# Optimization experiments

Measured on AMD Instinct MI355X. Metric: run time of the kernel, lower is better.

Reference implementation:

```python
import jax, jax.numpy as jnp
import numpy as np

B, C, H, W = 8, 128, 96, 96
E = 8           # num_experts
K = 3           # active_experts
HID = 4 * C     # hidden dim of each expert (hidden_ratio=4)


def _conv1x1(x, w, b):
    # x: [B,C,H,W], w: [O,C], b: [O] -> [B,O,H,W]
    return jnp.einsum('bchw,oc->bohw', x, w) + b[None, :, None, None]


def setup_inputs() -> dict:
    key = jax.random.key(0)
    ks = jax.random.split(key, 12)
    s = lambda k, shape, fan_in: jax.random.normal(k, shape, jnp.float32) * (1.0 / np.sqrt(fan_in))
    return {
        'x':   jax.random.normal(ks[0], (B, C, H, W), jnp.float32),
        # shared expert: Conv2d(C->HID,1x1), GELU, Conv2d(HID->C,1x1)
        'sw1': s(ks[1], (HID, C), C),   'sb1': jnp.zeros((HID,), jnp.float32),
        'sw2': s(ks[2], (C, HID), HID), 'sb2': jnp.zeros((C,), jnp.float32),
        # router gate: Conv2d(C->E,1x1)
        'gw':  s(ks[3], (E, C), C),     'gb':  jnp.zeros((E,), jnp.float32),
        # stacked routed experts
        'ew1': s(ks[4], (E, HID, C), C),   'eb1': jnp.zeros((E, HID), jnp.float32),
        'ew2': s(ks[5], (E, C, HID), HID), 'eb2': jnp.zeros((E, C), jnp.float32),
    }


def reference(x, sw1, sb1, sw2, sb2, gw, gb, ew1, eb1, ew2, eb2):
    # shared expert (exact GELU, matching torch nn.GELU default)
    h_s = jax.nn.gelu(_conv1x1(x, sw1, sb1), approximate=False)
    shared_out = _conv1x1(h_s, sw2, sb2)

    # router: softmax over expert dim, top-k, renormalize
    logits = _conv1x1(x, gw, gb)                      # [B,E,H,W]
    scores = jax.nn.softmax(logits, axis=1)           # [B,E,H,W]
    s_last = jnp.transpose(scores, (0, 2, 3, 1))      # [B,H,W,E]
    topk_probs, topk_idx = jax.lax.top_k(s_last, K)   # [B,H,W,K]
    topk_probs = topk_probs / jnp.sum(topk_probs, axis=-1, keepdims=True)

    # expert_mask[b,e,h,w]: routing weight for expert e at location (scatter-equivalent)
    onehot = jax.nn.one_hot(topk_idx, E, dtype=x.dtype)        # [B,H,W,K,E]
    mask = jnp.einsum('bhwke,bhwk->behw', onehot, topk_probs)  # [B,E,H,W]

    # dense compute of all experts (faithful to original), masked combine
    h = jax.nn.gelu(jnp.einsum('bchw,eoc->beohw', x, ew1)
                    + eb1[None, :, :, None, None], approximate=False)  # [B,E,HID,H,W]
    y = jnp.einsum('beohw,eco->bechw', h, ew2) + eb2[None, :, :, None, None]
    moe_out = jnp.einsum('bechw,behw->bchw', y, mask)

    # load-balancing aux loss
    mean_prob = jnp.mean(scores, axis=(0, 2, 3))               # [E]
    mean_load = jnp.mean(jnp.sum(onehot, axis=3), axis=(0, 1, 2))  # [E]
    aux_loss = E * jnp.sum(mean_prob * mean_load)

    return (x + shared_out + moe_out, aux_loss)
```

## Files before the change

### kernel.cpp

```cpp
#include <hip/hip_runtime.h>


typedef __bf16 bf16x8 __attribute__((ext_vector_type(8)));
typedef unsigned short u16x8 __attribute__((ext_vector_type(8)));
typedef float f32x4 __attribute__((ext_vector_type(4)));

#define HWP 9216
#define NPIX 73728
#define LDX 136
#define LDH 136
#define LXP 68
#define MAXSLOTS 77312
#define MAXTILES 1208
#define NSH 16

__device__ __forceinline__ unsigned short f2bf(float f) {
    unsigned u = __float_as_uint(f);
    u += 0x7fffu + ((u >> 16) & 1u);
    return (unsigned short)(u >> 16);
}

__device__ __forceinline__ unsigned pk_bf16(float a, float b) {
    return (unsigned)f2bf(a) | ((unsigned)f2bf(b) << 16);
}

__device__ __forceinline__ float bf2f(unsigned short h) {
    return __uint_as_float((unsigned)h << 16);
}

__device__ __forceinline__ float fast_gelu(float x) {
    float x2 = x * x;
    float u = x * fmaf(0.0356774081f, x2, 0.7978845608f);
    float e = __builtin_amdgcn_exp2f(u * 2.8853900818f);
    float r = __builtin_amdgcn_rcpf(e + 1.0f);
    float t = fmaf(-2.0f, r, 1.0f);
    float s = 0.5f * x;
    return fmaf(s, t, s);
}

__device__ __forceinline__ f32x4 mfma16(u16x8 a, u16x8 b, f32x4 c) {
    return __builtin_amdgcn_mfma_f32_16x16x32_bf16(
        __builtin_bit_cast(bf16x8, a), __builtin_bit_cast(bf16x8, b), c, 0, 0, 0);
}

__global__ __launch_bounds__(256) void router_fused(
    const float* __restrict__ x, const float* __restrict__ gw,
    const float* __restrict__ gb,
    const float* __restrict__ sw1, const float* __restrict__ sw2,
    const float* __restrict__ ew1, const float* __restrict__ ew2,
    unsigned short* __restrict__ wbf,
    unsigned short* __restrict__ xT,
    int* __restrict__ pixmask, float* __restrict__ pixw3,
    int* __restrict__ pixaux,
    int* __restrict__ bincount, float* __restrict__ accum)
{
    __shared__ float gws[1024];
    __shared__ float xls[128 * LXP];
    __shared__ float part[4 * 64 * 8];

    const int tid = threadIdx.x;
    const int blk = blockIdx.x;
    const int shadow = blk & (NSH - 1);

    {
        int i = blk * 256 + tid;
        #pragma unroll
        for (int j = 0; j < 4; ++j) {
            float v;
            if (i < 65536) v = sw1[i];
            else if (i < 131072) v = sw2[i - 65536];
            else if (i < 655360) v = ew1[i - 131072];
            else v = ew2[i - 655360];
            wbf[i] = f2bf(v);
            i += 1152 * 256;
        }
    }

    for (int i = tid; i < 1024; i += 256) gws[i] = gw[i];

    const int b = blk / 144;
    const int p0 = (blk - b * 144) * 64;
    const float* xb = x + (size_t)b * 128 * HWP + p0;

    #pragma unroll
    for (int j = 0; j < 8; ++j) {
        int id4 = j * 256 + tid;
        int c = id4 >> 4;
        int g = id4 & 15;
        f32x4 v = *(const f32x4*)(xb + (size_t)c * HWP + g * 4);
        *(f32x4*)&xls[c * LXP + g * 4] = v;
    }
    __syncthreads();

    const int p = tid & 63, q = tid >> 6;
    {
        float lg[8];
        #pragma unroll
        for (int e = 0; e < 8; ++e) lg[e] = 0.f;
        #pragma unroll
        for (int k = 0; k < 32; ++k) {
            int c = q * 32 + k;
            float xv = xls[c * LXP + p];
            #pragma unroll
            for (int e = 0; e < 8; ++e) lg[e] = fmaf(xv, gws[e * 128 + c], lg[e]);
        }
        #pragma unroll
        for (int e = 0; e < 8; ++e) part[(q * 64 + p) * 8 + e] = lg[e];
    }
    __syncthreads();

    if (tid < 64) {
        const int gp = b * HWP + p0 + tid;
        float l2[8];
        #pragma unroll
        for (int e = 0; e < 8; ++e)
            l2[e] = gb[e] + part[tid * 8 + e] + part[(64 + tid) * 8 + e]
                  + part[(128 + tid) * 8 + e] + part[(192 + tid) * 8 + e];
        float mx = l2[0];
        #pragma unroll
        for (int e = 1; e < 8; ++e) mx = fmaxf(mx, l2[e]);
        float pr[8]; float s = 0.f;
        #pragma unroll
        for (int e = 0; e < 8; ++e) { pr[e] = __expf(l2[e] - mx); s += pr[e]; }
        float sinv = __builtin_amdgcn_rcpf(s);
        #pragma unroll
        for (int e = 0; e < 8; ++e) pr[e] *= sinv;

        unsigned chosen = 0; float topsum = 0.f;
        for (int k = 0; k < 3; ++k) {
            int best = 0; float bv = -1.f;
            #pragma unroll
            for (int e = 0; e < 8; ++e) {
                bool ok = !((chosen >> e) & 1u) && pr[e] > bv;
                bv = ok ? pr[e] : bv;
                best = ok ? e : best;
            }
            chosen |= 1u << best;
            topsum += bv;
        }
        float tinv = __builtin_amdgcn_rcpf(topsum);

        pixmask[gp] = (int)chosen;
        {
            int j = 0;
            #pragma unroll
            for (int e = 0; e < 8; ++e)
                if ((chosen >> e) & 1u) { pixw3[gp * 3 + j] = pr[e] * tinv; ++j; }
        }

        unsigned long long eq = ~0ull;
        #pragma unroll
        for (int bit = 0; bit < 8; ++bit) {
            unsigned long long bb = __ballot((chosen >> bit) & 1u);
            eq &= ((chosen >> bit) & 1u) ? bb : ~bb;
        }
        const unsigned long long lowmask = (tid == 0) ? 0ull : (~0ull >> (64 - tid));
        int rank = __popcll(eq & lowmask);
        int cnt = __popcll(eq);
        int leader = __ffsll((unsigned long long)eq) - 1;
        int off_val = 0;
        if (rank == 0) off_val = atomicAdd(&bincount[shadow * 256 + (int)chosen], cnt);
        int binoff = __shfl(off_val, leader);
        pixaux[gp] = binoff + rank;

        #pragma unroll
        for (int e = 0; e < 8; ++e) {
            float v = pr[e];
            float c2 = ((chosen >> e) & 1u) ? 1.f : 0.f;
            #pragma unroll
            for (int off = 32; off > 0; off >>= 1) {
                v += __shfl_down(v, off);
                c2 += __shfl_down(c2, off);
            }
            if (tid == 0) {
                atomicAdd(&accum[shadow * 16 + e], v);
                atomicAdd(&accum[shadow * 16 + 8 + e], c2);
            }
        }
    }

    {
        const int pp = tid >> 2, qq = tid & 3;
        unsigned short* dst = xT + ((size_t)(blk * 64 + pp)) * 128 + qq * 32;
        #pragma unroll
        for (int j = 0; j < 4; ++j) {
            const int c0 = qq * 32 + j * 8;
            uint4 wv;
            wv.x = pk_bf16(xls[(c0 + 0) * LXP + pp], xls[(c0 + 1) * LXP + pp]);
            wv.y = pk_bf16(xls[(c0 + 2) * LXP + pp], xls[(c0 + 3) * LXP + pp]);
            wv.z = pk_bf16(xls[(c0 + 4) * LXP + pp], xls[(c0 + 5) * LXP + pp]);
            wv.w = pk_bf16(xls[(c0 + 6) * LXP + pp], xls[(c0 + 7) * LXP + pp]);
            *(uint4*)(dst + j * 8) = wv;
        }
    }
}

__global__ __launch_bounds__(256) void fill_bins(
    const int* __restrict__ bincount, const int* __restrict__ pixmask,
    int* __restrict__ idx, int* __restrict__ pixaux,
    int* __restrict__ tileMask, int* __restrict__ tileBase,
    int* __restrict__ ntiles)
{
    __shared__ int spc[256], snt[256], bb[256];
    __shared__ int sbase[NSH][256];
    const int tid = threadIdx.x;
    int c = 0;
    #pragma unroll
    for (int s = 0; s < NSH; ++s) {
        sbase[s][tid] = c;
        c += bincount[s * 256 + tid];
    }
    const int nt = (c + 63) >> 6;
    const int pc = nt << 6;
    spc[tid] = pc; snt[tid] = nt;
    __syncthreads();
    #pragma unroll
    for (int off = 1; off < 256; off <<= 1) {
        int a = (tid >= off) ? spc[tid - off] : 0;
        int d = (tid >= off) ? snt[tid - off] : 0;
        __syncthreads();
        spc[tid] += a; snt[tid] += d;
        __syncthreads();
    }
    const int base = spc[tid] - pc;
    bb[tid] = base;
    if (blockIdx.x == 0) {
        const int tstart = snt[tid] - nt;
        for (int j = 0; j < nt; ++j) {
            tileMask[tstart + j] = tid;
            tileBase[tstart + j] = base + (j << 6);
        }
        if (tid == 255) ntiles[0] = snt[255];
    }
    __syncthreads();

    const int gp = blockIdx.x * 256 + tid;
    int mask = pixmask[gp];
    int shadow = (gp >> 6) & (NSH - 1);
    int slot = bb[mask] + sbase[shadow][mask] + pixaux[gp];
    idx[slot] = gp;
    pixaux[gp] = slot;
}

__global__ __launch_bounds__(256, 3) void moe_sparse(
    const unsigned short* __restrict__ xT, const int* __restrict__ idx,
    const float* __restrict__ pixw3,
    const int* __restrict__ tileMask, const int* __restrict__ tileBase,
    const int* __restrict__ ntiles,
    const unsigned short* __restrict__ wbf,
    const float* __restrict__ sb1, const float* __restrict__ sb2,
    const float* __restrict__ eb1, const float* __restrict__ eb2,
    unsigned short* __restrict__ outT)
{
    __shared__ unsigned short xs[64 * LDX];
    __shared__ unsigned short hs[64 * LDH];
    __shared__ float wls[64 * 4];

    const int t = blockIdx.x;
    if (t >= ntiles[0]) return;
    const int mask = tileMask[t];
    const int base = tileBase[t];
    const int tid = threadIdx.x;

    {
        const int p = tid >> 2, q = tid & 3;
        const int gp = idx[base + p];
        const unsigned short* src = xT + (size_t)gp * 128 + q * 32;
        unsigned short* dst = &xs[p * LDX + q * 32];
        #pragma unroll
        for (int j = 0; j < 4; ++j)
            *(u16x8*)(dst + j * 8) = *(const u16x8*)(src + j * 8);
        if (q == 0) {
            wls[p * 4 + 0] = pixw3[gp * 3 + 0];
            wls[p * 4 + 1] = pixw3[gp * 3 + 1];
            wls[p * 4 + 2] = pixw3[gp * 3 + 2];
        }
    }
    __syncthreads();

    int el[3];
    { int n = 0;
      #pragma unroll
      for (int e = 0; e < 8; ++e) if ((mask >> e) & 1) { if (n < 3) el[n] = e; ++n; } }

    const int wave = tid >> 6;
    const int lr = tid & 15;
    const int lq = (tid >> 4) & 3;

    const f32x4 vzero = {0.f, 0.f, 0.f, 0.f};
    f32x4 fin[2][4];
    #pragma unroll
    for (int t2 = 0; t2 < 2; ++t2)
        #pragma unroll
        for (int nt2 = 0; nt2 < 4; ++nt2) fin[t2][nt2] = vzero;

    for (int pass = 0; pass < 4; ++pass) {
        const unsigned short* w1; const unsigned short* w2;
        const float* b1; const float* b2;
        if (pass == 0) { w1 = wbf; b1 = sb1; w2 = wbf + 65536; b2 = sb2; }
        else {
            int e = el[pass - 1];
            w1 = wbf + 131072 + (size_t)e * (512 * 128);  b1 = eb1 + e * 512;
            w2 = wbf + 655360 + (size_t)e * (128 * 512);  b2 = eb2 + e * 128;
        }

        f32x4 tmp[2][4];
        #pragma unroll
        for (int t2 = 0; t2 < 2; ++t2)
            #pragma unroll
            for (int nt2 = 0; nt2 < 4; ++nt2) tmp[t2][nt2] = vzero;

        for (int chunk = 0; chunk < 4; ++chunk) {
            u16x8 w1f[2][4];
            #pragma unroll
            for (int t2 = 0; t2 < 2; ++t2) {
                const int hid0 = chunk * 128 + wave * 32 + t2 * 16;
                const u16x8* wr = (const u16x8*)(w1 + (size_t)(hid0 + lr) * 128) + lq;
                #pragma unroll
                for (int ks = 0; ks < 4; ++ks) w1f[t2][ks] = wr[ks * 4];
            }
            f32x4 acc[2][4];
            #pragma unroll
            for (int t2 = 0; t2 < 2; ++t2)
                #pragma unroll
                for (int nt2 = 0; nt2 < 4; ++nt2) acc[t2][nt2] = vzero;
            #pragma unroll
            for (int ks = 0; ks < 4; ++ks) {
                #pragma unroll
                for (int nt2 = 0; nt2 < 4; ++nt2) {
                    u16x8 xf = *(const u16x8*)&xs[(nt2 * 16 + lr) * LDX + ks * 32 + lq * 8];
                    acc[0][nt2] = mfma16(w1f[0][ks], xf, acc[0][nt2]);
                    acc[1][nt2] = mfma16(w1f[1][ks], xf, acc[1][nt2]);
                }
            }
            #pragma unroll
            for (int t2 = 0; t2 < 2; ++t2) {
                const int hl = wave * 32 + t2 * 16 + lq * 4;
                const f32x4 b1v = *(const f32x4*)&b1[chunk * 128 + hl];
                #pragma unroll
                for (int nt2 = 0; nt2 < 4; ++nt2) {
                    float g0 = fast_gelu(acc[t2][nt2][0] + b1v[0]);
                    float g1 = fast_gelu(acc[t2][nt2][1] + b1v[1]);
                    float g2 = fast_gelu(acc[t2][nt2][2] + b1v[2]);
                    float g3 = fast_gelu(acc[t2][nt2][3] + b1v[3]);
                    uint2 wv = {pk_bf16(g0, g1), pk_bf16(g2, g3)};
                    *(uint2*)&hs[(nt2 * 16 + lr) * LDH + hl] = wv;
                }
            }
            __syncthreads();
            u16x8 w2f[2][4];
            #pragma unroll
            for (int t2 = 0; t2 < 2; ++t2) {
                const int c0 = wave * 32 + t2 * 16;
                const u16x8* wr = (const u16x8*)(w2 + (size_t)(c0 + lr) * 512 + chunk * 128) + lq;
                #pragma unroll
                for (int ks = 0; ks < 4; ++ks) w2f[t2][ks] = wr[ks * 4];
            }
            #pragma unroll
            for (int ks = 0; ks < 4; ++ks) {
                #pragma unroll
                for (int nt2 = 0; nt2 < 4; ++nt2) {
                    u16x8 hb = *(const u16x8*)&hs[(nt2 * 16 + lr) * LDH + ks * 32 + lq * 8];
                    tmp[0][nt2] = mfma16(w2f[0][ks], hb, tmp[0][nt2]);
                    tmp[1][nt2] = mfma16(w2f[1][ks], hb, tmp[1][nt2]);
                }
            }
            __syncthreads();
        }
        float wtv[4];
        #pragma unroll
        for (int nt2 = 0; nt2 < 4; ++nt2)
            wtv[nt2] = (pass == 0) ? 1.0f : wls[(nt2 * 16 + lr) * 4 + (pass - 1)];
        #pragma unroll
        for (int t2 = 0; t2 < 2; ++t2) {
            const f32x4 b2v = *(const f32x4*)&b2[wave * 32 + t2 * 16 + lq * 4];
            #pragma unroll
            for (int nt2 = 0; nt2 < 4; ++nt2)
                #pragma unroll
                for (int r = 0; r < 4; ++r)
                    fin[t2][nt2][r] += wtv[nt2] * (tmp[t2][nt2][r] + b2v[r]);
        }
    }

    #pragma unroll
    for (int t2 = 0; t2 < 2; ++t2)
        #pragma unroll
        for (int nt2 = 0; nt2 < 4; ++nt2) {
            unsigned short* dst = outT + ((size_t)(base + nt2 * 16 + lr)) * 128
                                + wave * 32 + t2 * 16 + lq * 4;
            uint2 wv = {pk_bf16(fin[t2][nt2][0], fin[t2][nt2][1]),
                        pk_bf16(fin[t2][nt2][2], fin[t2][nt2][3])};
            *(uint2*)dst = wv;
        }
}

__global__ __launch_bounds__(256) void final_add(
    const float* __restrict__ x, const unsigned short* __restrict__ outT,
    const int* __restrict__ pixslot, const float* __restrict__ accum,
    float* __restrict__ out)
{
    if (blockIdx.x == 0 && threadIdx.x == 0) {
        float a16[16];
        #pragma unroll
        for (int i = 0; i < 16; ++i) {
            float s = 0.f;
            #pragma unroll
            for (int sh = 0; sh < NSH; ++sh) s += accum[sh * 16 + i];
            a16[i] = s;
        }
        float aux = 0.f;
        #pragma unroll
        for (int e = 0; e < 8; ++e) aux += a16[e] * a16[8 + e];
        out[9437184] = 8.0f * aux / ((float)NPIX * (float)NPIX);
    }
    __shared__ unsigned short ts[64 * 133];
    const int blk = blockIdx.x;
    const int b = blk / 144;
    const int p0 = (blk - b * 144) * 64;
    const int tid = threadIdx.x;
    {
        const int p = tid >> 2, q = tid & 3;
        const int slot = pixslot[blk * 64 + p];
        const unsigned short* src = outT + (size_t)slot * 128 + q * 32;
        unsigned short* dst = &ts[p * 133 + q * 32];
        #pragma unroll
        for (int j = 0; j < 4; ++j)
            *(u16x8*)(dst + j * 8) = *(const u16x8*)(src + j * 8);
    }
    __syncthreads();
    const int pl = tid & 63, cq = tid >> 6;
    const float* xb = x + (size_t)b * 128 * HWP + p0;
    float* ob = out + (size_t)b * 128 * HWP + p0;
    #pragma unroll
    for (int c0 = 0; c0 < 128; c0 += 4) {
        int c = c0 + cq;
        ob[(size_t)c * HWP + pl] = xb[(size_t)c * HWP + pl] + bf2f(ts[pl * 133 + c]);
    }
}

extern "C" void kernel_launch(void* const* d_in, const int* in_sizes, int n_in,
                              void* d_out, int out_size, void* d_ws, size_t ws_size,
                              hipStream_t stream)
{
    const float* x   = (const float*)d_in[0];
    const float* sw1 = (const float*)d_in[1];
    const float* sb1 = (const float*)d_in[2];
    const float* sw2 = (const float*)d_in[3];
    const float* sb2 = (const float*)d_in[4];
    const float* gw  = (const float*)d_in[5];
    const float* gb  = (const float*)d_in[6];
    const float* ew1 = (const float*)d_in[7];
    const float* eb1 = (const float*)d_in[8];
    const float* ew2 = (const float*)d_in[9];
    const float* eb2 = (const float*)d_in[10];
    float* out = (float*)d_out;
    char* ws = (char*)d_ws;

    const size_t o_wbf     = 0;
    const size_t o_xT      = 2359296;
    const size_t o_outT    = o_xT + 18874368;
    const size_t o_pixmask = o_outT + 19791872;
    const size_t o_pixw3   = o_pixmask + 294912;
    const size_t o_pixaux  = o_pixw3 + 884736;
    const size_t o_tmask   = o_pixaux + 294912;
    const size_t o_tbase   = o_tmask + 4864;
    const size_t o_idx     = o_tbase + 4864;
    const size_t o_cnt     = o_idx + 309248;
    const size_t o_ntiles  = o_cnt + 16384;
    const size_t o_accum   = o_ntiles + 16;
    const size_t MEMSET_SZ = 309248 + 16384 + 16 + 1024;

    unsigned short* wbf  = (unsigned short*)(ws + o_wbf);
    unsigned short* xT   = (unsigned short*)(ws + o_xT);
    unsigned short* outT = (unsigned short*)(ws + o_outT);
    int* pixmask  = (int*)(ws + o_pixmask);
    float* pixw3  = (float*)(ws + o_pixw3);
    int* pixaux   = (int*)(ws + o_pixaux);
    int* tmask    = (int*)(ws + o_tmask);
    int* tbase    = (int*)(ws + o_tbase);
    int* idx      = (int*)(ws + o_idx);
    int* bincount = (int*)(ws + o_cnt);
    int* ntiles   = (int*)(ws + o_ntiles);
    float* accum  = (float*)(ws + o_accum);

    (void)hipMemsetAsync(ws + o_idx, 0, MEMSET_SZ, stream);
    router_fused<<<1152, 256, 0, stream>>>(x, gw, gb, sw1, sw2, ew1, ew2, wbf,
                                           xT, pixmask, pixw3, pixaux, bincount, accum);
    fill_bins<<<288, 256, 0, stream>>>(bincount, pixmask, idx, pixaux,
                                       tmask, tbase, ntiles);
    moe_sparse<<<MAXTILES, 256, 0, stream>>>(xT, idx, pixw3, tmask, tbase, ntiles,
        wbf, sb1, sb2, eb1, eb2, outT);
    final_add<<<1152, 256, 0, stream>>>(x, outT, pixaux, accum, out);
}
```

Before: 338.1 us.

## Double-buffer hidden tile and prefetch next W1 fragments across flattened chunk loop

Flattens the pass/chunk loops into a single 16-iteration loop and double-buffers the shared hidden-activation tile, so one of the two barriers per chunk can be dropped. It also prefetches the next chunk's W1 register fragments while the current GEMM and GELU run, hiding global weight-load latency. The cost is extra LDS for the second hidden buffer and more live registers, which could reduce occupancy under the 3-blocks-per-SM launch bound.

```diff
diff --git a/kernel.cpp b/kernel.cpp
--- a/kernel.cpp
+++ b/kernel.cpp
@@ -253,7 +253,7 @@
     unsigned short* __restrict__ outT)
 {
     __shared__ unsigned short xs[64 * LDX];
-    __shared__ unsigned short hs[64 * LDH];
+    __shared__ unsigned short hs[2][64 * LDH];
     __shared__ float wls[64 * 4];
 
     const int t = blockIdx.x;
@@ -287,6 +287,23 @@
     const int lr = tid & 15;
     const int lq = (tid >> 4) & 3;
 
+    const unsigned short* const w1t0 = wbf;
+    const unsigned short* const w1t1 = wbf + 131072 + (size_t)el[0] * 65536;
+    const unsigned short* const w1t2 = wbf + 131072 + (size_t)el[1] * 65536;
+    const unsigned short* const w1t3 = wbf + 131072 + (size_t)el[2] * 65536;
+    const unsigned short* const w2t0 = wbf + 65536;
+    const unsigned short* const w2t1 = wbf + 655360 + (size_t)el[0] * 65536;
+    const unsigned short* const w2t2 = wbf + 655360 + (size_t)el[1] * 65536;
+    const unsigned short* const w2t3 = wbf + 655360 + (size_t)el[2] * 65536;
+    const float* const b1t0 = sb1;
+    const float* const b1t1 = eb1 + el[0] * 512;
+    const float* const b1t2 = eb1 + el[1] * 512;
+    const float* const b1t3 = eb1 + el[2] * 512;
+    const float* const b2t0 = sb2;
+    const float* const b2t1 = eb2 + el[0] * 128;
+    const float* const b2t2 = eb2 + el[1] * 128;
+    const float* const b2t3 = eb2 + el[2] * 128;
+
     const f32x4 vzero = {0.f, 0.f, 0.f, 0.f};
     f32x4 fin[2][4];
     #pragma unroll
@@ -294,45 +311,66 @@
         #pragma unroll
         for (int nt2 = 0; nt2 < 4; ++nt2) fin[t2][nt2] = vzero;
 
-    for (int pass = 0; pass < 4; ++pass) {
-        const unsigned short* w1; const unsigned short* w2;
-        const float* b1; const float* b2;
-        if (pass == 0) { w1 = wbf; b1 = sb1; w2 = wbf + 65536; b2 = sb2; }
-        else {
-            int e = el[pass - 1];
-            w1 = wbf + 131072 + (size_t)e * (512 * 128);  b1 = eb1 + e * 512;
-            w2 = wbf + 655360 + (size_t)e * (128 * 512);  b2 = eb2 + e * 128;
-        }
-
-        f32x4 tmp[2][4];
+    f32x4 tmp[2][4];
+    u16x8 w1f[2][4];
+    u16x8 w2f[2][4];
+
+    #pragma unroll
+    for (int t2 = 0; t2 < 2; ++t2) {
+        const int hid0 = wave * 32 + t2 * 16;
+        const u16x8* wr = (const u16x8*)(w1t0 + (size_t)(hid0 + lr) * 128) + lq;
+        #pragma unroll
+        for (int ks = 0; ks < 4; ++ks) w1f[t2][ks] = wr[ks * 4];
+    }
+
+    for (int cc = 0; cc < 16; ++cc) {
+        const int pass = cc >> 2;
+        const int chunk = cc & 3;
+        unsigned short* hsb = &hs[cc & 1][0];
+
+        f32x4 acc[2][4];
         #pragma unroll
         for (int t2 = 0; t2 < 2; ++t2)
             #pragma unroll
-            for (int nt2 = 0; nt2 < 4; ++nt2) tmp[t2][nt2] = vzero;
-
-        for (int chunk = 0; chunk < 4; ++chunk) {
-            u16x8 w1f[2][4];
+            for (int nt2 = 0; nt2 < 4; ++nt2) acc[t2][nt2] = vzero;
+        #pragma unroll
+        for (int ks = 0; ks < 4; ++ks) {
+            #pragma unroll
+            for (int nt2 = 0; nt2 < 4; ++nt2) {
+                u16x8 xf = *(const u16x8*)&xs[(nt2 * 16 + lr) * LDX + ks * 32 + lq * 8];
+                acc[0][nt2] = mfma16(w1f[0][ks], xf, acc[0][nt2]);
+                acc[1][nt2] = mfma16(w1f[1][ks], xf, acc[1][nt2]);
+            }
+        }
+
+        {
+            const unsigned short* w2 = (pass == 0) ? w2t0 : (pass == 1) ? w2t1
+                                     : (pass == 2) ? w2t2 : w2t3;
             #pragma unroll
             for (int t2 = 0; t2 < 2; ++t2) {
-                const int hid0 = chunk * 128 + wave * 32 + t2 * 16;
-                const u16x8* wr = (const u16x8*)(w1 + (size_t)(hid0 + lr) * 128) + lq;
+                const int c0 = wave * 32 + t2 * 16;
+                const u16x8* wr = (const u16x8*)(w2 + (size_t)(c0 + lr) * 512 + chunk * 128) + lq;
+                #pragma unroll
+                for (int ks = 0; ks < 4; ++ks) w2f[t2][ks] = wr[ks * 4];
+            }
+        }
+        if (cc < 15) {
+            const int ccn = cc + 1;
+            const int pn = ccn >> 2, cn = ccn & 3;
+            const unsigned short* w1n = (pn == 0) ? w1t0 : (pn == 1) ? w1t1
+                                      : (pn == 2) ? w1t2 : w1t3;
+            #pragma unroll
+            for (int t2 = 0; t2 < 2; ++t2) {
+                const int hid0 = cn * 128 + wave * 32 + t2 * 16;
+                const u16x8* wr = (const u16x8*)(w1n + (size_t)(hid0 + lr) * 128) + lq;
                 #pragma unroll
                 for (int ks = 0; ks < 4; ++ks) w1f[t2][ks] = wr[ks * 4];
             }
-            f32x4 acc[2][4];
-            #pragma unroll
-            for (int t2 = 0; t2 < 2; ++t2)
-                #pragma unroll
-                for (int nt2 = 0; nt2 < 4; ++nt2) acc[t2][nt2] = vzero;
-            #pragma unroll
-            for (int ks = 0; ks < 4; ++ks) {
-                #pragma unroll
-                for (int nt2 = 0; nt2 < 4; ++nt2) {
-                    u16x8 xf = *(const u16x8*)&xs[(nt2 * 16 + lr) * LDX + ks * 32 + lq * 8];
-                    acc[0][nt2] = mfma16(w1f[0][ks], xf, acc[0][nt2]);
-                    acc[1][nt2] = mfma16(w1f[1][ks], xf, acc[1][nt2]);
-                }
-            }
+        }
+
+        {
+            const float* b1 = (pass == 0) ? b1t0 : (pass == 1) ? b1t1
+                            : (pass == 2) ? b1t2 : b1t3;
             #pragma unroll
             for (int t2 = 0; t2 < 2; ++t2) {
                 const int hl = wave * 32 + t2 * 16 + lq * 4;
@@ -344,41 +382,45 @@
                     float g2 = fast_gelu(acc[t2][nt2][2] + b1v[2]);
                     float g3 = fast_gelu(acc[t2][nt2][3] + b1v[3]);
                     uint2 wv = {pk_bf16(g0, g1), pk_bf16(g2, g3)};
-                    *(uint2*)&hs[(nt2 * 16 + lr) * LDH + hl] = wv;
+                    *(uint2*)&hsb[(nt2 * 16 + lr) * LDH + hl] = wv;
                 }
             }
-            __syncthreads();
-            u16x8 w2f[2][4];
+        }
+
+        __syncthreads();
+
+        if (chunk == 0) {
+            #pragma unroll
+            for (int t2 = 0; t2 < 2; ++t2)
+                #pragma unroll
+                for (int nt2 = 0; nt2 < 4; ++nt2) tmp[t2][nt2] = vzero;
+        }
+        #pragma unroll
+        for (int ks = 0; ks < 4; ++ks) {
+            #pragma unroll
+            for (int nt2 = 0; nt2 < 4; ++nt2) {
+                u16x8 hb = *(const u16x8*)&hsb[(nt2 * 16 + lr) * LDH + ks * 32 + lq * 8];
+                tmp[0][nt2] = mfma16(w2f[0][ks], hb, tmp[0][nt2]);
+                tmp[1][nt2] = mfma16(w2f[1][ks], hb, tmp[1][nt2]);
+            }
+        }
+
+        if (chunk == 3) {
+            const float* b2 = (pass == 0) ? b2t0 : (pass == 1) ? b2t1
+                            : (pass == 2) ? b2t2 : b2t3;
+            float wtv[4];
+            #pragma unroll
+            for (int nt2 = 0; nt2 < 4; ++nt2)
+                wtv[nt2] = (pass == 0) ? 1.0f : wls[(nt2 * 16 + lr) * 4 + (pass - 1)];
             #pragma unroll
             for (int t2 = 0; t2 < 2; ++t2) {
-                const int c0 = wave * 32 + t2 * 16;
-                const u16x8* wr = (const u16x8*)(w2 + (size_t)(c0 + lr) * 512 + chunk * 128) + lq;
+                const f32x4 b2v = *(const f32x4*)&b2[wave * 32 + t2 * 16 + lq * 4];
                 #pragma unroll
-                for (int ks = 0; ks < 4; ++ks) w2f[t2][ks] = wr[ks * 4];
-            }
-            #pragma unroll
-            for (int ks = 0; ks < 4; ++ks) {
-                #pragma unroll
-                for (int nt2 = 0; nt2 < 4; ++nt2) {
-                    u16x8 hb = *(const u16x8*)&hs[(nt2 * 16 + lr) * LDH + ks * 32 + lq * 8];
-                    tmp[0][nt2] = mfma16(w2f[0][ks], hb, tmp[0][nt2]);
-                    tmp[1][nt2] = mfma16(w2f[1][ks], hb, tmp[1][nt2]);
-                }
-            }
-            __syncthreads();
-        }
-        float wtv[4];
-        #pragma unroll
-        for (int nt2 = 0; nt2 < 4; ++nt2)
-            wtv[nt2] = (pass == 0) ? 1.0f : wls[(nt2 * 16 + lr) * 4 + (pass - 1)];
-        #pragma unroll
-        for (int t2 = 0; t2 < 2; ++t2) {
-            const f32x4 b2v = *(const f32x4*)&b2[wave * 32 + t2 * 16 + lq * 4];
-            #pragma unroll
-            for (int nt2 = 0; nt2 < 4; ++nt2)
-                #pragma unroll
-                for (int r = 0; r < 4; ++r)
-                    fin[t2][nt2][r] += wtv[nt2] * (tmp[t2][nt2][r] + b2v[r]);
+                for (int nt2 = 0; nt2 < 4; ++nt2)
+                    #pragma unroll
+                    for (int r = 0; r < 4; ++r)
+                        fin[t2][nt2][r] += wtv[nt2] * (tmp[t2][nt2][r] + b2v[r]);
+            }
         }
     }
 
```

Measured after the change: 410.7 us. +21.5%, slower.
